# Kernel optimization log

Hardware: AMD Instinct MI355X
Metric: run time of the kernel (lower is better)

Reference implementation:

```python
import jax, jax.numpy as jnp
import numpy as np

T, Q, D, NH, L = 6, 300, 256, 8, 4
DH = D // NH
PC, PT = 2, 1
WT = T - 1
P = PC + WT * PT
DFF = 1024
SHAPES = [(128, 128), (64, 64), (32, 32), (16, 16)]
S_PER_FRAME = sum(h * w for h, w in SHAPES)


def _layer_norm(x, g, b, eps=1e-5):
    mu = jnp.mean(x, -1, keepdims=True)
    v = jnp.mean(jnp.square(x - mu), -1, keepdims=True)
    return (x - mu) * jax.lax.rsqrt(v + eps) * g + b


def _bilinear(vlh, loc, frame_pt, Hl, Wl):
    # vlh: [NH, T*Hl*Wl, DH]; loc: [TQ, NH, P, 2] normalized; frame_pt: np [TQ, P] int32
    x = loc[..., 0] * Wl - 0.5
    y = loc[..., 1] * Hl - 0.5
    x0 = jnp.floor(x)
    y0 = jnp.floor(y)
    fx = x - x0
    fy = y - y0
    x0 = x0.astype(jnp.int32)
    y0 = y0.astype(jnp.int32)
    fbase = (frame_pt[:, None, :] * np.int32(Hl * Wl)).astype(np.int32)  # [TQ,1,P]
    acc = 0.0
    for dy, wy in ((0, 1.0 - fy), (1, fy)):
        for dx, wx in ((0, 1.0 - fx), (1, fx)):
            xi = x0 + dx
            yi = y0 + dy
            ok = (xi >= 0) & (xi < Wl) & (yi >= 0) & (yi < Hl)
            idx = fbase + jnp.clip(yi, 0, Hl - 1) * Wl + jnp.clip(xi, 0, Wl - 1)  # [TQ,NH,P]
            g = jax.vmap(lambda v, i: v[i], in_axes=(0, 1), out_axes=0)(vlh, idx)  # [NH,TQ,P,DH]
            w = wy * wx * ok  # [TQ,NH,P]
            acc = acc + g * jnp.transpose(w, (1, 0, 2))[..., None]
    return acc  # [NH,TQ,P,DH]


def _forward(src, tgt_masks, query_pos, reference_points, src_valid_ratios,
             Wq, bq, Wk, bk, Wv, bv, Wo, bo, norm2_g, norm2_b,
             Wval, bval, Woff, boff, Watt, batt, Wout, bout, norm1_g, norm1_b,
             W1, b1, W2, b2, norm3_g, norm3_b,
             src_spatial_shapes, src_level_start_index):
    shapes = np.asarray(src_spatial_shapes)
    # ---- self-attention across frames (seq=T, batch=Q, as in nn.MultiheadAttention) ----
    qk_in = tgt_masks + query_pos  # [T,Q,D]
    qh = (qk_in @ Wq.T + bq).reshape(T, Q, NH, DH)
    kh = (qk_in @ Wk.T + bk).reshape(T, Q, NH, DH)
    vh = (tgt_masks @ Wv.T + bv).reshape(T, Q, NH, DH)
    logits = jnp.einsum('iqhd,jqhd->qhij', qh, kh) * (1.0 / np.sqrt(DH))
    attn = jax.nn.softmax(logits, -1)
    sa = jnp.einsum('qhij,jqhd->iqhd', attn, vh).reshape(T, Q, D) @ Wo.T + bo
    tgt = _layer_norm(tgt_masks + sa, norm2_g, norm2_b)  # [T,Q,D]

    tgt = tgt.reshape(T * Q, D)
    query = tgt + query_pos.reshape(T * Q, D)

    # ---- current-frame and temporal (same-instance) reference points ----
    ref = reference_points.reshape(T * Q, 2)
    vr0 = src_valid_ratios[0]  # [L,2]
    ref_curr = ref[:, None, :] * vr0[None]  # [TQ,L,2]
    others = np.array([[f for f in range(T) if f != t] for t in range(T)], np.int32)  # [T,WT]
    ref_oth = reference_points[others]  # [T,WT,Q,2]
    ref_oth = jnp.transpose(ref_oth, (0, 2, 1, 3)).reshape(T * Q, WT, 2)
    ref_temp = ref_oth[:, :, None, :] * vr0[None, None]  # [TQ,WT,L,2]

    fid = np.repeat(np.arange(T, dtype=np.int32), Q)  # [TQ]
    oth_fid = np.repeat(others, Q, axis=0)  # [TQ,WT]
    frame_pt = np.concatenate([np.tile(fid[:, None], (1, PC)), oth_fid], axis=1).astype(np.int32)  # [TQ,P]

    # ---- temporal multi-scale deformable cross-attention ----
    value = (src[0] @ Wval.T + bval).reshape(-1, NH, DH)  # [T*S,NH,DH]
    off = (query @ Woff.T + boff).reshape(T * Q, NH, L, P, 2)
    att = jax.nn.softmax((query @ Watt.T + batt).reshape(T * Q, NH, L * P), -1)
    att = att.reshape(T * Q, NH, L, P)

    out = jnp.zeros((T * Q, NH, DH), src.dtype)
    start = 0
    for l in range(L):
        Hl, Wl = int(shapes[l, 0]), int(shapes[l, 1])
        n = T * Hl * Wl
        vlh = value[start:start + n].transpose(1, 0, 2)  # [NH, T*Hl*Wl, DH]
        start += n
        bc = jnp.tile(ref_curr[:, l][:, None, :], (1, PC, 1))  # [TQ,PC,2]
        bt = ref_temp[:, :, l, :]  # [TQ,WT,2]
        base = jnp.concatenate([bc, bt], 1)[:, None]  # [TQ,1,P,2]
        loc = base + off[:, :, l] / jnp.array([Wl, Hl], jnp.float32)  # [TQ,NH,P,2]
        sampled = _bilinear(vlh, loc, frame_pt, Hl, Wl)  # [NH,TQ,P,DH]
        out = out + jnp.einsum('nqpd,qnp->qnd', sampled, att[:, :, l])
    cross = out.reshape(T * Q, D) @ Wout.T + bout
    tgt = _layer_norm(tgt + cross, norm1_g, norm1_b)

    # ---- FFN ----
    h = jax.nn.relu(tgt @ W1.T + b1)
    tgt = _layer_norm(tgt + h @ W2.T + b2, norm3_g, norm3_b)
    return tgt.reshape(T, Q, D)


def setup_inputs() -> dict:
    key = jax.random.key(0)
    ki = iter(jax.random.split(key, 48))

    def rn(shape, s=1.0):
        return jax.random.normal(next(ki), shape, jnp.float32) * s

    return {
        'src': rn((1, T * S_PER_FRAME, D)),
        'tgt_masks': rn((T, Q, D)),
        'query_pos': rn((T, Q, D), 0.5),
        'reference_points': jax.random.uniform(next(ki), (T, Q, 2), jnp.float32, 0.25, 0.75),
        'src_valid_ratios': jax.random.uniform(next(ki), (T, L, 2), jnp.float32, 0.9, 1.0),
        'src_spatial_shapes': jnp.array(SHAPES, jnp.int32),
        'src_level_start_index': jnp.array(np.cumsum([0] + [T * h * w for h, w in SHAPES[:-1]]), jnp.int32),
        'Wq': rn((D, D), 0.02), 'bq': jnp.zeros((D,)),
        'Wk': rn((D, D), 0.02), 'bk': jnp.zeros((D,)),
        'Wv': rn((D, D), 0.02), 'bv': jnp.zeros((D,)),
        'Wo': rn((D, D), 0.02), 'bo': jnp.zeros((D,)),
        'norm2_g': jnp.ones((D,)), 'norm2_b': jnp.zeros((D,)),
        'Wval': rn((D, D), 0.02), 'bval': jnp.zeros((D,)),
        'Woff': rn((NH * L * P * 2, D), 0.01), 'boff': rn((NH * L * P * 2,), 0.1),
        'Watt': rn((NH * L * P, D), 0.01), 'batt': jnp.zeros((NH * L * P,)),
        'Wout': rn((D, D), 0.02), 'bout': jnp.zeros((D,)),
        'norm1_g': jnp.ones((D,)), 'norm1_b': jnp.zeros((D,)),
        'W1': rn((DFF, D), 0.02), 'b1': jnp.zeros((DFF,)),
        'W2': rn((D, DFF), 0.02), 'b2': jnp.zeros((D,)),
        'norm3_g': jnp.ones((D,)), 'norm3_b': jnp.zeros((D,)),
    }


def reference(src, tgt_masks, query_pos, reference_points, src_valid_ratios,
              src_spatial_shapes, src_level_start_index,
              Wq, bq, Wk, bk, Wv, bv, Wo, bo, norm2_g, norm2_b,
              Wval, bval, Woff, boff, Watt, batt, Wout, bout, norm1_g, norm1_b,
              W1, b1, W2, b2, norm3_g, norm3_b):
    return _forward(src, tgt_masks, query_pos, reference_points, src_valid_ratios,
                    Wq, bq, Wk, bk, Wv, bv, Wo, bo, norm2_g, norm2_b,
                    Wval, bval, Woff, boff, Watt, batt, Wout, bout, norm1_g, norm1_b,
                    W1, b1, W2, b2, norm3_g, norm3_b,
                    src_spatial_shapes, src_level_start_index)
```

## Files before the change

### kernel.cpp

```cpp
#include <hip/hip_runtime.h>
#include <hip/hip_bf16.h>

#define T_ 6
#define Q_ 300
#define TQ 1800
#define D_ 256
#define NH_ 8
#define DH_ 32
#define L_ 4
#define P_ 7
#define DFF_ 1024
#define NV 130560
#define NVB 1020
#define QKVB 174

#define OW_VAL 0
#define OW_Q   65536
#define OW_K   131072
#define OW_V   196608
#define OW_O   262144
#define OW_OUT 327680
#define OW_OFF 393216
#define OW_ATT 507904
#define OW_1   565248
#define OW_2   827392
#define OW_TOT 1089536

typedef __attribute__((ext_vector_type(8))) short bf16x8;
typedef __attribute__((ext_vector_type(4))) float f32x4;
typedef __attribute__((ext_vector_type(8))) unsigned short u16x8;
typedef __attribute__((ext_vector_type(4))) unsigned short u16x4;

__device__ inline float bf2f(unsigned short s) {
    union { unsigned u; float f; } v; v.u = ((unsigned)s) << 16;
    return v.f;
}
__device__ inline unsigned short f2b_rn(float f) {
    __hip_bfloat16 h = __float2bfloat16(f);
    union { __hip_bfloat16 h; unsigned short u; } c; c.h = h; return c.u;
}

__global__ __launch_bounds__(256) void wcvt_kernel(
    const float* __restrict__ s0, const float* __restrict__ s1,
    const float* __restrict__ s2, const float* __restrict__ s3,
    const float* __restrict__ s4, const float* __restrict__ s5,
    const float* __restrict__ s6, const float* __restrict__ s7,
    const float* __restrict__ s8, const float* __restrict__ s9,
    unsigned short* __restrict__ dst)
{
    int idx4 = blockIdx.x * blockDim.x + threadIdx.x;
    const int total4 = OW_TOT / 4;
    for (; idx4 < total4; idx4 += gridDim.x * blockDim.x) {
        int e = idx4 * 4;
        const float* s; int off;
        if      (e < OW_Q)   { s = s0; off = e; }
        else if (e < OW_K)   { s = s1; off = e - OW_Q; }
        else if (e < OW_V)   { s = s2; off = e - OW_K; }
        else if (e < OW_O)   { s = s3; off = e - OW_V; }
        else if (e < OW_OUT) { s = s4; off = e - OW_O; }
        else if (e < OW_OFF) { s = s5; off = e - OW_OUT; }
        else if (e < OW_ATT) { s = s6; off = e - OW_OFF; }
        else if (e < OW_1)   { s = s7; off = e - OW_ATT; }
        else if (e < OW_2)   { s = s8; off = e - OW_1; }
        else                 { s = s9; off = e - OW_2; }
        f32x4 v = *(const f32x4*)(s + off);
        u16x4 o;
#pragma unroll
        for (int j = 0; j < 4; j++) o[j] = f2b_rn(v[j]);
        *(u16x4*)(dst + e) = o;
    }
}

__global__ __launch_bounds__(512) void mega1_kernel(
    const float* __restrict__ A, const unsigned short* __restrict__ wbf,
    const float* __restrict__ bias,
    unsigned short* __restrict__ out,
    const float* __restrict__ tgtm, const float* __restrict__ qpos,
    const float* __restrict__ bq, const float* __restrict__ bk,
    const float* __restrict__ bv,
    float* __restrict__ qh, float* __restrict__ kh, float* __restrict__ vh)
{
    __shared__ unsigned short Ws[256 * 256];
    __shared__ float As[2][128 * 32];

    int tid = threadIdx.x;
    int wave = tid >> 6, lane = tid & 63;
    int r = lane & 15, g = lane >> 4;

    if (blockIdx.x < NVB) {
        int m0 = blockIdx.x * 128;
        int rs = r & 7;

#pragma unroll
        for (int j = 0; j < 16; j++) {
            int o = wave * 16 + j;
            int col = o * 2 + (lane >> 5);
            int slot = lane & 31;
            const unsigned short* s =
                wbf + OW_VAL + (size_t)col * 256 + (size_t)((slot ^ (col & 7)) * 8);
            __builtin_amdgcn_global_load_lds(
                (const __attribute__((address_space(1))) void*)s,
                (__attribute__((address_space(3))) void*)&Ws[o * 512], 16, 0, 0);
        }

#define DMA_A(ks, b) do { \
        int o_ = wave * 2; \
        int ro_ = o_ * 8 + (lane >> 3); \
        int kg_ = (lane & 7) ^ (lane >> 3); \
        const float* s0_ = A + (size_t)(m0 + ro_) * 256 + (ks) * 32 + kg_ * 4; \
        const float* s1_ = s0_ + 8 * 256; \
        __builtin_amdgcn_global_load_lds( \
            (const __attribute__((address_space(1))) void*)s0_, \
            (__attribute__((address_space(3))) void*)&As[b][o_ * 256], 16, 0, 0); \
        __builtin_amdgcn_global_load_lds( \
            (const __attribute__((address_space(1))) void*)s1_, \
            (__attribute__((address_space(3))) void*)&As[b][(o_ + 1) * 256], 16, 0, 0); \
    } while (0)

        DMA_A(0, 0);
        __syncthreads();

        int wm = wave >> 2, wn = wave & 3;
        f32x4 acc[4][4] = {};

#define PHASE(ks, b) do { \
        bf16x8 af[4]; \
        _Pragma("unroll") \
        for (int mi = 0; mi < 4; mi++) { \
            int row_ = wm * 64 + mi * 16 + r; \
            f32x4 lo_ = *(const f32x4*)&As[b][row_ * 32 + (((g * 2) ^ rs) << 2)]; \
            f32x4 hi_ = *(const f32x4*)&As[b][row_ * 32 + (((g * 2 + 1) ^ rs) << 2)]; \
            _Pragma("unroll") \
            for (int j = 0; j < 4; j++) { \
                af[mi][j] = (short)f2b_rn(lo_[j]); \
                af[mi][4 + j] = (short)f2b_rn(hi_[j]); \
            } \
        } \
        _Pragma("unroll") \
        for (int ni = 0; ni < 4; ni++) { \
            int col_ = wn * 64 + ni * 16 + r; \
            bf16x8 bfr = *(const bf16x8*)&Ws[col_ * 256 + ((((ks) * 4 + g) ^ rs) << 3)]; \
            _Pragma("unroll") \
            for (int mi = 0; mi < 4; mi++) \
                acc[mi][ni] = __builtin_amdgcn_mfma_f32_16x16x32_bf16(af[mi], bfr, acc[mi][ni], 0, 0, 0); \
        } \
    } while (0)

        DMA_A(1, 1); PHASE(0, 0); __syncthreads();
        DMA_A(2, 0); PHASE(1, 1); __syncthreads();
        DMA_A(3, 1); PHASE(2, 0); __syncthreads();
        DMA_A(4, 0); PHASE(3, 1); __syncthreads();
        DMA_A(5, 1); PHASE(4, 0); __syncthreads();
        DMA_A(6, 0); PHASE(5, 1); __syncthreads();
        DMA_A(7, 1); PHASE(6, 0); __syncthreads();
        PHASE(7, 1);
#undef PHASE
#undef DMA_A

#pragma unroll
        for (int ni = 0; ni < 4; ni++) {
            int col = wn * 64 + ni * 16 + r;
            float bv2 = bias[col];
#pragma unroll
            for (int mi = 0; mi < 4; mi++) {
#pragma unroll
                for (int rr = 0; rr < 4; rr++) {
                    int row = m0 + wm * 64 + mi * 16 + g * 4 + rr;
                    out[(size_t)row * 256 + col] = f2b_rn(acc[mi][ni][rr] + bv2);
                }
            }
        }
    } else {
        int b = blockIdx.x - NVB;
        int bmx = b % 29, by = b / 29;
        int wm = wave >> 2, wn = wave & 3;
        int m0 = bmx * 64 + wm * 32;
        int n0g = by * 128 + wn * 32;
        int seg = n0g >> 8;
        int n0 = n0g & 255;
        const unsigned short* Wp = wbf + (seg == 0 ? OW_Q : (seg == 1 ? OW_K : OW_V));
        const float* bp = (seg == 0) ? bq : (seg == 1) ? bk : bv;
        float* outp = (seg == 0) ? qh : (seg == 1) ? kh : vh;
        bool add2 = (seg < 2);

        f32x4 acc[2][2] = {};
#pragma unroll
        for (int kk = 0; kk < 256; kk += 32) {
            int kbase = kk + g * 8;
            bf16x8 af[2], wf[2];
#pragma unroll
            for (int mi = 0; mi < 2; mi++) {
                int row = m0 + mi * 16 + r; if (row >= TQ) row = TQ - 1;
                const float* ap = tgtm + (size_t)row * 256 + kbase;
                f32x4 lo = *(const f32x4*)ap, hi = *(const f32x4*)(ap + 4);
                if (add2) {
                    const float* ap2 = qpos + (size_t)row * 256 + kbase;
                    lo += *(const f32x4*)ap2; hi += *(const f32x4*)(ap2 + 4);
                }
#pragma unroll
                for (int j = 0; j < 4; j++) { af[mi][j] = (short)f2b_rn(lo[j]); af[mi][4 + j] = (short)f2b_rn(hi[j]); }
            }
#pragma unroll
            for (int ni = 0; ni < 2; ni++) {
                int col = n0 + ni * 16 + r;
                wf[ni] = *(const bf16x8*)&Wp[(size_t)col * 256 + kbase];
            }
#pragma unroll
            for (int mi = 0; mi < 2; mi++)
#pragma unroll
                for (int ni = 0; ni < 2; ni++)
                    acc[mi][ni] = __builtin_amdgcn_mfma_f32_16x16x32_bf16(af[mi], wf[ni], acc[mi][ni], 0, 0, 0);
        }
#pragma unroll
        for (int mi = 0; mi < 2; mi++)
#pragma unroll
            for (int ni = 0; ni < 2; ni++) {
                int col = n0 + ni * 16 + r;
                float bv2 = bp[col];
#pragma unroll
                for (int rr = 0; rr < 4; rr++) {
                    int row = m0 + mi * 16 + g * 4 + rr;
                    if (row < TQ) outp[(size_t)row * 256 + col] = acc[mi][ni][rr] + bv2;
                }
            }
    }
}

__global__ __launch_bounds__(256) void attn_wo_ln2_kernel(
    const float* __restrict__ qh, const float* __restrict__ kh,
    const float* __restrict__ vh, const float* __restrict__ tgtm,
    const float* __restrict__ qpos, const unsigned short* __restrict__ wbf,
    const float* __restrict__ bo, const float* __restrict__ n2g,
    const float* __restrict__ n2b,
    float* __restrict__ tgt1, float* __restrict__ query)
{
    int q = blockIdx.x;
    int tid = threadIdx.x;
    __shared__ float qs[T_][D_], ks_[T_][D_], vs[T_][D_];
    __shared__ unsigned short po[16][268];
    __shared__ float sa32[16][264];

#pragma unroll
    for (int i = 0; i < T_; i++) {
        size_t base = (size_t)(i * Q_ + q) * D_ + tid;
        qs[i][tid] = qh[base]; ks_[i][tid] = kh[base]; vs[i][tid] = vh[base];
    }
    __syncthreads();

    const float scale = 0.17677669529663687f;
    float lg[T_][T_];
#pragma unroll
    for (int i = 0; i < T_; i++)
#pragma unroll
        for (int j = 0; j < T_; j++) {
            float p = qs[i][tid] * ks_[j][tid];
#pragma unroll
            for (int m = 16; m >= 1; m >>= 1) p += __shfl_xor(p, m, 32);
            lg[i][j] = p * scale;
        }
#pragma unroll
    for (int i = 0; i < T_; i++) {
        float mx = lg[i][0];
#pragma unroll
        for (int j = 1; j < T_; j++) mx = fmaxf(mx, lg[i][j]);
        float w[T_]; float sum = 0.f;
#pragma unroll
        for (int j = 0; j < T_; j++) { w[j] = __expf(lg[i][j] - mx); sum += w[j]; }
        float inv = 1.f / sum;
        float a = 0.f;
#pragma unroll
        for (int j = 0; j < T_; j++) a += w[j] * inv * vs[j][tid];
        po[i][tid] = f2b_rn(a);
    }
#pragma unroll
    for (int i = T_; i < 16; i++) po[i][tid] = 0;
    __syncthreads();

    const unsigned short* Wo = wbf + OW_O;
    int wn = tid >> 6, lane = tid & 63;
    int r = lane & 15, g = lane >> 4;
    f32x4 acc[4] = {};
#pragma unroll
    for (int ksx = 0; ksx < 8; ksx++) {
        int kbase = ksx * 32 + g * 8;
        bf16x8 af = *(const bf16x8*)&po[r][kbase];
        bf16x8 bfr[4];
#pragma unroll
        for (int ni = 0; ni < 4; ni++)
            bfr[ni] = *(const bf16x8*)&Wo[(size_t)(wn * 64 + ni * 16 + r) * 256 + kbase];
#pragma unroll
        for (int ni = 0; ni < 4; ni++)
            acc[ni] = __builtin_amdgcn_mfma_f32_16x16x32_bf16(af, bfr[ni], acc[ni], 0, 0, 0);
    }
#pragma unroll
    for (int ni = 0; ni < 4; ni++) {
        int col = wn * 64 + ni * 16 + r;
#pragma unroll
        for (int rr = 0; rr < 4; rr++) {
            int row = g * 4 + rr;
            if (row < T_)
                sa32[row][col] = acc[ni][rr] + bo[col] + tgtm[(size_t)(row * Q_ + q) * 256 + col];
        }
    }
    __syncthreads();

    int rl = tid >> 3, l8 = tid & 7;
    if (rl < T_) {
        float s = 0.f, s2 = 0.f;
#pragma unroll
        for (int c = 0; c < 256; c += 8) {
            float v = sa32[rl][c + l8];
            s += v; s2 += v * v;
        }
#pragma unroll
        for (int m = 4; m >= 1; m >>= 1) { s += __shfl_xor(s, m, 64); s2 += __shfl_xor(s2, m, 64); }
        float mu = s * (1.f / 256.f);
        float var = s2 * (1.f / 256.f) - mu * mu;
        float rs = rsqrtf(var + 1e-5f);
        size_t grow = (size_t)(rl * Q_ + q) * 256;
#pragma unroll
        for (int c = 0; c < 256; c += 8) {
            int cc = c + l8;
            float y = (sa32[rl][cc] - mu) * rs * n2g[cc] + n2b[cc];
            tgt1[grow + cc] = y;
            query[grow + cc] = y + qpos[grow + cc];
        }
    }
}

__global__ __launch_bounds__(256) void offatt_kernel(
    const float* __restrict__ query, const unsigned short* __restrict__ wbf,
    const float* __restrict__ boff, const float* __restrict__ batt,
    float* __restrict__ offb, float* __restrict__ attl)
{
    int wave = threadIdx.x >> 6;
    int lane = threadIdx.x & 63;
    int wm = wave >> 1, wn = wave & 1;
    int m0 = blockIdx.x * 64 + wm * 32;
    int n0g = blockIdx.y * 64 + wn * 32;
    int seg = (n0g >= 448);
    int n0 = seg ? (n0g - 448) : n0g;
    int Nloc = seg ? 224 : 448;
    const unsigned short* W = wbf + (seg ? OW_ATT : OW_OFF);
    const float* bias = seg ? batt : boff;
    float* out = seg ? attl : offb;
    int r = lane & 15, g = lane >> 4;

    f32x4 acc[2][2] = {};
#pragma unroll
    for (int kk = 0; kk < 256; kk += 32) {
        int kbase = kk + g * 8;
        bf16x8 af[2], wf[2];
#pragma unroll
        for (int mi = 0; mi < 2; mi++) {
            int row = m0 + mi * 16 + r; if (row >= TQ) row = TQ - 1;
            const float* ap = query + (size_t)row * 256 + kbase;
            f32x4 lo = *(const f32x4*)ap, hi = *(const f32x4*)(ap + 4);
#pragma unroll
            for (int j = 0; j < 4; j++) { af[mi][j] = (short)f2b_rn(lo[j]); af[mi][4 + j] = (short)f2b_rn(hi[j]); }
        }
#pragma unroll
        for (int ni = 0; ni < 2; ni++) {
            int col = n0 + ni * 16 + r; if (col >= Nloc) col = Nloc - 1;
            wf[ni] = *(const bf16x8*)&W[(size_t)col * 256 + kbase];
        }
#pragma unroll
        for (int mi = 0; mi < 2; mi++)
#pragma unroll
            for (int ni = 0; ni < 2; ni++)
                acc[mi][ni] = __builtin_amdgcn_mfma_f32_16x16x32_bf16(af[mi], wf[ni], acc[mi][ni], 0, 0, 0);
    }
#pragma unroll
    for (int mi = 0; mi < 2; mi++)
#pragma unroll
        for (int ni = 0; ni < 2; ni++) {
            int col = n0 + ni * 16 + r;
            if (col < Nloc) {
                float bv2 = bias[col];
#pragma unroll
                for (int rr = 0; rr < 4; rr++) {
                    int row = m0 + mi * 16 + g * 4 + rr;
                    if (row < TQ) out[(size_t)row * Nloc + col] = acc[mi][ni][rr] + bv2;
                }
            }
        }
}

__global__ __launch_bounds__(256) void sample_kernel(
    const unsigned short* __restrict__ value, const float* __restrict__ attl,
    const float* __restrict__ off, const float* __restrict__ refp,
    const float* __restrict__ vr, float* __restrict__ out)
{
    int q = blockIdx.x;
    int tid = threadIdx.x;
    int d = tid & 31, h = tid >> 5;
    int t = q / Q_, qq = q - t * Q_;

    __shared__ float aw[NH_][28], ofx[NH_][28], ofy[NH_][28];

    float lgv = (d < 28) ? attl[(size_t)q * 224 + h * 28 + d] : -1e30f;
    float mx = lgv;
#pragma unroll
    for (int m = 16; m >= 1; m >>= 1) mx = fmaxf(mx, __shfl_xor(mx, m, 32));
    float e = (d < 28) ? __expf(lgv - mx) : 0.f;
    float s = e;
#pragma unroll
    for (int m = 16; m >= 1; m >>= 1) s += __shfl_xor(s, m, 32);
    if (d < 28) {
        aw[h][d] = e / s;
        ofx[h][d] = off[(size_t)q * 448 + h * 56 + d * 2 + 0];
        ofy[h][d] = off[(size_t)q * 448 + h * 56 + d * 2 + 1];
    }
    __syncthreads();

    const int WLs[4] = {128, 64, 32, 16};
    const int LST[4] = {0, 98304, 122880, 129024};

    float acc = 0.f;
#pragma unroll
    for (int l = 0; l < L_; l++) {
        const int Wl = WLs[l], Hl = WLs[l];
        const int lst = LST[l];
        float vrx = vr[l * 2 + 0], vry = vr[l * 2 + 1];
#pragma unroll
        for (int p = 0; p < P_; p++) {
            int f = (p < 2) ? t : (((p - 2) < t) ? (p - 2) : (p - 1));
            float rx = refp[(size_t)(f * Q_ + qq) * 2 + 0];
            float ry = refp[(size_t)(f * Q_ + qq) * 2 + 1];
            int ip = l * 7 + p;
            float x = rx * vrx * (float)Wl + ofx[h][ip] - 0.5f;
            float y = ry * vry * (float)Hl + ofy[h][ip] - 0.5f;
            float x0f = floorf(x), y0f = floorf(y);
            float fx = x - x0f, fy = y - y0f;
            int x0 = (int)x0f, y0 = (int)y0f;
            int fbase = lst + f * Hl * Wl;
            float a = aw[h][ip];
#pragma unroll
            for (int dy = 0; dy < 2; dy++) {
                int yi = y0 + dy;
                float wy = dy ? fy : 1.f - fy;
                int yc = min(max(yi, 0), Hl - 1);
                bool oky = (yi >= 0) && (yi < Hl);
#pragma unroll
                for (int dx = 0; dx < 2; dx++) {
                    int xi = x0 + dx;
                    float wx = dx ? fx : 1.f - fx;
                    int xc = min(max(xi, 0), Wl - 1);
                    bool ok = oky && (xi >= 0) && (xi < Wl);
                    float v = bf2f(value[((size_t)(fbase + yc * Wl + xc)) * D_ + h * DH_ + d]);
                    acc += a * (ok ? (wy * wx) : 0.f) * v;
                }
            }
        }
    }
    out[(size_t)q * D_ + tid] = acc;
}

__global__ __launch_bounds__(256) void tail_kernel(
    const float* __restrict__ samp, const unsigned short* __restrict__ wbf,
    const float* __restrict__ bout, const float* __restrict__ tgt1,
    const float* __restrict__ n1g, const float* __restrict__ n1b,
    const float* __restrict__ b1, const float* __restrict__ b2,
    const float* __restrict__ n3g, const float* __restrict__ n3b,
    float* __restrict__ dout)
{
    __shared__ float c32[16][264];
    __shared__ float t232[16][264];
    __shared__ unsigned short t2bf[16][268];
    __shared__ unsigned short hbf[16][1036];

    int tid = threadIdx.x;
    int wn = tid >> 6, lane = tid & 63;
    int r = lane & 15, g = lane >> 4;
    int m0 = blockIdx.x * 16;

    const unsigned short* Wout = wbf + OW_OUT;
    const unsigned short* W1 = wbf + OW_1;
    const unsigned short* W2 = wbf + OW_2;

    {
        f32x4 acc[4] = {};
        int row = m0 + r; if (row >= TQ) row = TQ - 1;
#pragma unroll
        for (int ksx = 0; ksx < 8; ksx++) {
            int kbase = ksx * 32 + g * 8;
            const float* ap = samp + (size_t)row * 256 + kbase;
            f32x4 lo = *(const f32x4*)ap, hi = *(const f32x4*)(ap + 4);
            bf16x8 af;
#pragma unroll
            for (int j = 0; j < 4; j++) { af[j] = (short)f2b_rn(lo[j]); af[4 + j] = (short)f2b_rn(hi[j]); }
            bf16x8 bfr[4];
#pragma unroll
            for (int ni = 0; ni < 4; ni++)
                bfr[ni] = *(const bf16x8*)&Wout[(size_t)(wn * 64 + ni * 16 + r) * 256 + kbase];
#pragma unroll
            for (int ni = 0; ni < 4; ni++)
                acc[ni] = __builtin_amdgcn_mfma_f32_16x16x32_bf16(af, bfr[ni], acc[ni], 0, 0, 0);
        }
#pragma unroll
        for (int ni = 0; ni < 4; ni++) {
            int col = wn * 64 + ni * 16 + r;
            float bv = bout[col];
#pragma unroll
            for (int rr = 0; rr < 4; rr++) {
                int rowl = g * 4 + rr;
                int grow = m0 + rowl;
                float res = (grow < TQ) ? tgt1[(size_t)grow * 256 + col] : 0.f;
                c32[rowl][col] = acc[ni][rr] + bv + res;
            }
        }
    }
    __syncthreads();

    if (tid < 128) {
        int rl = tid >> 3, l8 = tid & 7;
        float s = 0.f, s2 = 0.f;
#pragma unroll
        for (int c = 0; c < 256; c += 8) {
            float v = c32[rl][c + l8];
            s += v; s2 += v * v;
        }
#pragma unroll
        for (int m = 4; m >= 1; m >>= 1) { s += __shfl_xor(s, m, 64); s2 += __shfl_xor(s2, m, 64); }
        float mu = s * (1.f / 256.f);
        float var = s2 * (1.f / 256.f) - mu * mu;
        float rs = rsqrtf(var + 1e-5f);
#pragma unroll
        for (int c = 0; c < 256; c += 8) {
            int cc = c + l8;
            float y = (c32[rl][cc] - mu) * rs * n1g[cc] + n1b[cc];
            t232[rl][cc] = y;
            t2bf[rl][cc] = f2b_rn(y);
        }
    }
    __syncthreads();

    {
        f32x4 acc[16] = {};
#pragma unroll
        for (int ksx = 0; ksx < 8; ksx++) {
            int kbase = ksx * 32 + g * 8;
            bf16x8 af = *(const bf16x8*)&t2bf[r][kbase];
#pragma unroll
            for (int ni = 0; ni < 16; ni++) {
                bf16x8 bfr = *(const bf16x8*)&W1[(size_t)(wn * 256 + ni * 16 + r) * 256 + kbase];
                acc[ni] = __builtin_amdgcn_mfma_f32_16x16x32_bf16(af, bfr, acc[ni], 0, 0, 0);
            }
        }
#pragma unroll
        for (int ni = 0; ni < 16; ni++) {
            int col = wn * 256 + ni * 16 + r;
            float bv = b1[col];
#pragma unroll
            for (int rr = 0; rr < 4; rr++) {
                int rowl = g * 4 + rr;
                hbf[rowl][col] = f2b_rn(fmaxf(acc[ni][rr] + bv, 0.f));
            }
        }
    }
    __syncthreads();

    {
        f32x4 acc[4] = {};
#pragma unroll
        for (int ksx = 0; ksx < 32; ksx++) {
            int kbase = ksx * 32 + g * 8;
            bf16x8 af = *(const bf16x8*)&hbf[r][kbase];
#pragma unroll
            for (int ni = 0; ni < 4; ni++) {
                bf16x8 bfr = *(const bf16x8*)&W2[(size_t)(wn * 64 + ni * 16 + r) * 1024 + kbase];
                acc[ni] = __builtin_amdgcn_mfma_f32_16x16x32_bf16(af, bfr, acc[ni], 0, 0, 0);
            }
        }
#pragma unroll
        for (int ni = 0; ni < 4; ni++) {
            int col = wn * 64 + ni * 16 + r;
            float bv = b2[col];
#pragma unroll
            for (int rr = 0; rr < 4; rr++) {
                int rowl = g * 4 + rr;
                c32[rowl][col] = acc[ni][rr] + bv + t232[rowl][col];
            }
        }
    }
    __syncthreads();

    if (tid < 128) {
        int rl = tid >> 3, l8 = tid & 7;
        int grow = m0 + rl;
        if (grow < TQ) {
            float s = 0.f, s2 = 0.f;
#pragma unroll
            for (int c = 0; c < 256; c += 8) {
                float v = c32[rl][c + l8];
                s += v; s2 += v * v;
            }
#pragma unroll
            for (int m = 4; m >= 1; m >>= 1) { s += __shfl_xor(s, m, 64); s2 += __shfl_xor(s2, m, 64); }
            float mu = s * (1.f / 256.f);
            float var = s2 * (1.f / 256.f) - mu * mu;
            float rs = rsqrtf(var + 1e-5f);
#pragma unroll
            for (int c = 0; c < 256; c += 8) {
                int cc = c + l8;
                dout[(size_t)grow * 256 + cc] = (c32[rl][cc] - mu) * rs * n3g[cc] + n3b[cc];
            }
        }
    }
}

extern "C" void kernel_launch(void* const* d_in, const int* in_sizes, int n_in,
                              void* d_out, int out_size, void* d_ws, size_t ws_size,
                              hipStream_t stream) {
    const float* src  = (const float*)d_in[0];
    const float* tgtm = (const float*)d_in[1];
    const float* qpos = (const float*)d_in[2];
    const float* refp = (const float*)d_in[3];
    const float* vr   = (const float*)d_in[4];
    const float* Wq = (const float*)d_in[7];  const float* bq = (const float*)d_in[8];
    const float* Wk = (const float*)d_in[9];  const float* bk = (const float*)d_in[10];
    const float* Wv = (const float*)d_in[11]; const float* bv = (const float*)d_in[12];
    const float* Wo = (const float*)d_in[13]; const float* bo = (const float*)d_in[14];
    const float* n2g = (const float*)d_in[15]; const float* n2b = (const float*)d_in[16];
    const float* Wval = (const float*)d_in[17]; const float* bval = (const float*)d_in[18];
    const float* Woff = (const float*)d_in[19]; const float* boff = (const float*)d_in[20];
    const float* Watt = (const float*)d_in[21]; const float* batt = (const float*)d_in[22];
    const float* Wout = (const float*)d_in[23]; const float* bout = (const float*)d_in[24];
    const float* n1g = (const float*)d_in[25]; const float* n1b = (const float*)d_in[26];
    const float* W1 = (const float*)d_in[27]; const float* b1 = (const float*)d_in[28];
    const float* W2 = (const float*)d_in[29]; const float* b2 = (const float*)d_in[30];
    const float* n3g = (const float*)d_in[31]; const float* n3b = (const float*)d_in[32];

    char* ws = (char*)d_ws;
    size_t o = 0;
    auto alloc = [&](size_t bytes) -> void* {
        void* p = ws + o; o += (bytes + 255) & ~(size_t)255; return p;
    };
    unsigned short* value = (unsigned short*)alloc((size_t)NV * D_ * 2);
    unsigned short* wbf   = (unsigned short*)alloc((size_t)OW_TOT * 2);
    float* qh     = (float*)alloc((size_t)TQ * D_ * 4);
    float* kh     = (float*)alloc((size_t)TQ * D_ * 4);
    float* vh     = (float*)alloc((size_t)TQ * D_ * 4);
    float* tgt1   = (float*)alloc((size_t)TQ * D_ * 4);
    float* query  = (float*)alloc((size_t)TQ * D_ * 4);
    float* offb   = (float*)alloc((size_t)TQ * 448 * 4);
    float* attl   = (float*)alloc((size_t)TQ * 224 * 4);
    float* samp   = (float*)alloc((size_t)TQ * D_ * 4);

    const int MT = (TQ + 63) / 64;

    wcvt_kernel<<<dim3((OW_TOT / 4 + 255) / 256), dim3(256), 0, stream>>>(
        Wval, Wq, Wk, Wv, Wo, Wout, Woff, Watt, W1, W2, wbf);

    mega1_kernel<<<dim3(NVB + QKVB), dim3(512), 0, stream>>>(
        src, wbf, bval, value, tgtm, qpos, bq, bk, bv, qh, kh, vh);

    attn_wo_ln2_kernel<<<dim3(Q_), dim3(256), 0, stream>>>(
        qh, kh, vh, tgtm, qpos, wbf, bo, n2g, n2b, tgt1, query);

    offatt_kernel<<<dim3(MT, 11), dim3(256), 0, stream>>>(query, wbf, boff, batt, offb, attl);

    sample_kernel<<<dim3(TQ), dim3(256), 0, stream>>>(value, attl, offb, refp, vr, samp);

    tail_kernel<<<dim3((TQ + 15) / 16), dim3(256), 0, stream>>>(
        samp, wbf, bout, tgt1, n1g, n1b, b1, b2, n3g, n3b, (float*)d_out);
}
```

Measured before the change: 191.1 us.

## Make value GEMM persistent over four tiles and fuse QKV projection into attention

Result: faster. 183.5 us (-4.0%).

```diff
diff --git a/kernel.cpp b/kernel.cpp
--- a/kernel.cpp
+++ b/kernel.cpp
@@ -11,8 +11,7 @@
 #define P_ 7
 #define DFF_ 1024
 #define NV 130560
-#define NVB 1020
-#define QKVB 174
+#define VBLK 255
 
 #define OW_VAL 0
 #define OW_Q   65536
@@ -71,14 +70,9 @@
     }
 }
 
-__global__ __launch_bounds__(512) void mega1_kernel(
+__global__ __launch_bounds__(512) void vgemm_kernel(
     const float* __restrict__ A, const unsigned short* __restrict__ wbf,
-    const float* __restrict__ bias,
-    unsigned short* __restrict__ out,
-    const float* __restrict__ tgtm, const float* __restrict__ qpos,
-    const float* __restrict__ bq, const float* __restrict__ bk,
-    const float* __restrict__ bv,
-    float* __restrict__ qh, float* __restrict__ kh, float* __restrict__ vh)
+    const float* __restrict__ bias, unsigned short* __restrict__ out)
 {
     __shared__ unsigned short Ws[256 * 256];
     __shared__ float As[2][128 * 32];
@@ -86,28 +80,26 @@
     int tid = threadIdx.x;
     int wave = tid >> 6, lane = tid & 63;
     int r = lane & 15, g = lane >> 4;
-
-    if (blockIdx.x < NVB) {
-        int m0 = blockIdx.x * 128;
-        int rs = r & 7;
-
-#pragma unroll
-        for (int j = 0; j < 16; j++) {
-            int o = wave * 16 + j;
-            int col = o * 2 + (lane >> 5);
-            int slot = lane & 31;
-            const unsigned short* s =
-                wbf + OW_VAL + (size_t)col * 256 + (size_t)((slot ^ (col & 7)) * 8);
-            __builtin_amdgcn_global_load_lds(
-                (const __attribute__((address_space(1))) void*)s,
-                (__attribute__((address_space(3))) void*)&Ws[o * 512], 16, 0, 0);
-        }
-
-#define DMA_A(ks, b) do { \
+    int rs = r & 7;
+    int base_m = blockIdx.x * 512;
+
+#pragma unroll
+    for (int j = 0; j < 16; j++) {
+        int o = wave * 16 + j;
+        int col = o * 2 + (lane >> 5);
+        int slot = lane & 31;
+        const unsigned short* s =
+            wbf + OW_VAL + (size_t)col * 256 + (size_t)((slot ^ (col & 7)) * 8);
+        __builtin_amdgcn_global_load_lds(
+            (const __attribute__((address_space(1))) void*)s,
+            (__attribute__((address_space(3))) void*)&Ws[o * 512], 16, 0, 0);
+    }
+
+#define DMA_A(tile, ks, b) do { \
         int o_ = wave * 2; \
         int ro_ = o_ * 8 + (lane >> 3); \
         int kg_ = (lane & 7) ^ (lane >> 3); \
-        const float* s0_ = A + (size_t)(m0 + ro_) * 256 + (ks) * 32 + kg_ * 4; \
+        const float* s0_ = A + (size_t)(base_m + (tile) * 128 + ro_) * 256 + (ks) * 32 + kg_ * 4; \
         const float* s1_ = s0_ + 8 * 256; \
         __builtin_amdgcn_global_load_lds( \
             (const __attribute__((address_space(1))) void*)s0_, \
@@ -117,125 +109,85 @@
             (__attribute__((address_space(3))) void*)&As[b][(o_ + 1) * 256], 16, 0, 0); \
     } while (0)
 
-        DMA_A(0, 0);
-        __syncthreads();
-
-        int wm = wave >> 2, wn = wave & 3;
-        f32x4 acc[4][4] = {};
-
-#define PHASE(ks, b) do { \
-        bf16x8 af[4]; \
-        _Pragma("unroll") \
-        for (int mi = 0; mi < 4; mi++) { \
-            int row_ = wm * 64 + mi * 16 + r; \
-            f32x4 lo_ = *(const f32x4*)&As[b][row_ * 32 + (((g * 2) ^ rs) << 2)]; \
-            f32x4 hi_ = *(const f32x4*)&As[b][row_ * 32 + (((g * 2 + 1) ^ rs) << 2)]; \
-            _Pragma("unroll") \
-            for (int j = 0; j < 4; j++) { \
-                af[mi][j] = (short)f2b_rn(lo_[j]); \
-                af[mi][4 + j] = (short)f2b_rn(hi_[j]); \
-            } \
-        } \
-        _Pragma("unroll") \
-        for (int ni = 0; ni < 4; ni++) { \
-            int col_ = wn * 64 + ni * 16 + r; \
-            bf16x8 bfr = *(const bf16x8*)&Ws[col_ * 256 + ((((ks) * 4 + g) ^ rs) << 3)]; \
-            _Pragma("unroll") \
-            for (int mi = 0; mi < 4; mi++) \
-                acc[mi][ni] = __builtin_amdgcn_mfma_f32_16x16x32_bf16(af[mi], bfr, acc[mi][ni], 0, 0, 0); \
-        } \
-    } while (0)
-
-        DMA_A(1, 1); PHASE(0, 0); __syncthreads();
-        DMA_A(2, 0); PHASE(1, 1); __syncthreads();
-        DMA_A(3, 1); PHASE(2, 0); __syncthreads();
-        DMA_A(4, 0); PHASE(3, 1); __syncthreads();
-        DMA_A(5, 1); PHASE(4, 0); __syncthreads();
-        DMA_A(6, 0); PHASE(5, 1); __syncthreads();
-        DMA_A(7, 1); PHASE(6, 0); __syncthreads();
-        PHASE(7, 1);
-#undef PHASE
+    DMA_A(0, 0, 0);
+    DMA_A(0, 1, 1);
+
+    int wm = wave >> 2, wn = wave & 3;
+    f32x4 acc[4][4] = {};
+
+    for (int p = 0; p < 32; ++p) {
+        if (p == 31) { asm volatile("s_waitcnt vmcnt(0)" ::: "memory"); }
+        else         { asm volatile("s_waitcnt vmcnt(2)" ::: "memory"); }
+        __builtin_amdgcn_s_barrier();
+        __builtin_amdgcn_sched_barrier(0);
+
+        int tile = p >> 3, ks = p & 7, b = p & 1;
+
+        {
+            bf16x8 af[4];
+#pragma unroll
+            for (int mi = 0; mi < 4; mi++) {
+                int row_ = wm * 64 + mi * 16 + r;
+                f32x4 lo_ = *(const f32x4*)&As[b][row_ * 32 + (((g * 2) ^ rs) << 2)];
+                f32x4 hi_ = *(const f32x4*)&As[b][row_ * 32 + (((g * 2 + 1) ^ rs) << 2)];
+#pragma unroll
+                for (int j = 0; j < 4; j++) {
+                    af[mi][j] = (short)f2b_rn(lo_[j]);
+                    af[mi][4 + j] = (short)f2b_rn(hi_[j]);
+                }
+            }
+#pragma unroll
+            for (int ni = 0; ni < 4; ni++) {
+                int col_ = wn * 64 + ni * 16 + r;
+                bf16x8 bfr = *(const bf16x8*)&Ws[col_ * 256 + (((ks * 4 + g) ^ rs) << 3)];
+#pragma unroll
+                for (int mi = 0; mi < 4; mi++)
+                    acc[mi][ni] = __builtin_amdgcn_mfma_f32_16x16x32_bf16(af[mi], bfr, acc[mi][ni], 0, 0, 0);
+            }
+        }
+
+        __builtin_amdgcn_s_barrier();
+        __builtin_amdgcn_sched_barrier(0);
+
+        int pn = p + 2;
+        if (pn < 32) DMA_A(pn >> 3, pn & 7, b);
+
+        if (ks == 7) {
+            int mbase = base_m + tile * 128 + wm * 64;
+#pragma unroll
+            for (int ni = 0; ni < 4; ni++) {
+                int col = wn * 64 + ni * 16 + r;
+                float bv2 = bias[col];
+#pragma unroll
+                for (int mi = 0; mi < 4; mi++) {
+#pragma unroll
+                    for (int rr = 0; rr < 4; rr++) {
+                        int row = mbase + mi * 16 + g * 4 + rr;
+                        out[(size_t)row * 256 + col] = f2b_rn(acc[mi][ni][rr] + bv2);
+                    }
+                }
+            }
+#pragma unroll
+            for (int mi = 0; mi < 4; mi++)
+#pragma unroll
+                for (int ni = 0; ni < 4; ni++)
+                    acc[mi][ni] = (f32x4){0.f, 0.f, 0.f, 0.f};
+        }
+    }
 #undef DMA_A
-
-#pragma unroll
-        for (int ni = 0; ni < 4; ni++) {
-            int col = wn * 64 + ni * 16 + r;
-            float bv2 = bias[col];
-#pragma unroll
-            for (int mi = 0; mi < 4; mi++) {
-#pragma unroll
-                for (int rr = 0; rr < 4; rr++) {
-                    int row = m0 + wm * 64 + mi * 16 + g * 4 + rr;
-                    out[(size_t)row * 256 + col] = f2b_rn(acc[mi][ni][rr] + bv2);
-                }
-            }
-        }
-    } else {
-        int b = blockIdx.x - NVB;
-        int bmx = b % 29, by = b / 29;
-        int wm = wave >> 2, wn = wave & 3;
-        int m0 = bmx * 64 + wm * 32;
-        int n0g = by * 128 + wn * 32;
-        int seg = n0g >> 8;
-        int n0 = n0g & 255;
-        const unsigned short* Wp = wbf + (seg == 0 ? OW_Q : (seg == 1 ? OW_K : OW_V));
-        const float* bp = (seg == 0) ? bq : (seg == 1) ? bk : bv;
-        float* outp = (seg == 0) ? qh : (seg == 1) ? kh : vh;
-        bool add2 = (seg < 2);
-
-        f32x4 acc[2][2] = {};
-#pragma unroll
-        for (int kk = 0; kk < 256; kk += 32) {
-            int kbase = kk + g * 8;
-            bf16x8 af[2], wf[2];
-#pragma unroll
-            for (int mi = 0; mi < 2; mi++) {
-                int row = m0 + mi * 16 + r; if (row >= TQ) row = TQ - 1;
-                const float* ap = tgtm + (size_t)row * 256 + kbase;
-                f32x4 lo = *(const f32x4*)ap, hi = *(const f32x4*)(ap + 4);
-                if (add2) {
-                    const float* ap2 = qpos + (size_t)row * 256 + kbase;
-                    lo += *(const f32x4*)ap2; hi += *(const f32x4*)(ap2 + 4);
-                }
-#pragma unroll
-                for (int j = 0; j < 4; j++) { af[mi][j] = (short)f2b_rn(lo[j]); af[mi][4 + j] = (short)f2b_rn(hi[j]); }
-            }
-#pragma unroll
-            for (int ni = 0; ni < 2; ni++) {
-                int col = n0 + ni * 16 + r;
-                wf[ni] = *(const bf16x8*)&Wp[(size_t)col * 256 + kbase];
-            }
-#pragma unroll
-            for (int mi = 0; mi < 2; mi++)
-#pragma unroll
-                for (int ni = 0; ni < 2; ni++)
-                    acc[mi][ni] = __builtin_amdgcn_mfma_f32_16x16x32_bf16(af[mi], wf[ni], acc[mi][ni], 0, 0, 0);
-        }
-#pragma unroll
-        for (int mi = 0; mi < 2; mi++)
-#pragma unroll
-            for (int ni = 0; ni < 2; ni++) {
-                int col = n0 + ni * 16 + r;
-                float bv2 = bp[col];
-#pragma unroll
-                for (int rr = 0; rr < 4; rr++) {
-                    int row = m0 + mi * 16 + g * 4 + rr;
-                    if (row < TQ) outp[(size_t)row * 256 + col] = acc[mi][ni][rr] + bv2;
-                }
-            }
-    }
 }
 
 __global__ __launch_bounds__(256) void attn_wo_ln2_kernel(
-    const float* __restrict__ qh, const float* __restrict__ kh,
-    const float* __restrict__ vh, const float* __restrict__ tgtm,
-    const float* __restrict__ qpos, const unsigned short* __restrict__ wbf,
-    const float* __restrict__ bo, const float* __restrict__ n2g,
-    const float* __restrict__ n2b,
+    const float* __restrict__ tgtm, const float* __restrict__ qpos,
+    const unsigned short* __restrict__ wbf,
+    const float* __restrict__ bq, const float* __restrict__ bk,
+    const float* __restrict__ bv, const float* __restrict__ bo,
+    const float* __restrict__ n2g, const float* __restrict__ n2b,
     float* __restrict__ tgt1, float* __restrict__ query)
 {
     int q = blockIdx.x;
     int tid = threadIdx.x;
+    __shared__ unsigned short xq[16][264], xv[16][264];
     __shared__ float qs[T_][D_], ks_[T_][D_], vs[T_][D_];
     __shared__ unsigned short po[16][268];
     __shared__ float sa32[16][264];
@@ -243,7 +195,48 @@
 #pragma unroll
     for (int i = 0; i < T_; i++) {
         size_t base = (size_t)(i * Q_ + q) * D_ + tid;
-        qs[i][tid] = qh[base]; ks_[i][tid] = kh[base]; vs[i][tid] = vh[base];
+        float tv = tgtm[base];
+        xq[i][tid] = f2b_rn(tv + qpos[base]);
+        xv[i][tid] = f2b_rn(tv);
+    }
+#pragma unroll
+    for (int i = T_; i < 16; i++) { xq[i][tid] = 0; xv[i][tid] = 0; }
+    __syncthreads();
+
+    int wn = tid >> 6, lane = tid & 63;
+    int r = lane & 15, g = lane >> 4;
+
+#pragma unroll
+    for (int proj = 0; proj < 3; proj++) {
+        const unsigned short* Wp = wbf + (proj == 0 ? OW_Q : (proj == 1 ? OW_K : OW_V));
+        const float* bp = (proj == 0) ? bq : (proj == 1) ? bk : bv;
+        f32x4 acc[4] = {};
+#pragma unroll
+        for (int ksx = 0; ksx < 8; ksx++) {
+            int kbase = ksx * 32 + g * 8;
+            bf16x8 af = (proj == 2) ? *(const bf16x8*)&xv[r][kbase]
+                                    : *(const bf16x8*)&xq[r][kbase];
+#pragma unroll
+            for (int ni = 0; ni < 4; ni++) {
+                bf16x8 wf = *(const bf16x8*)&Wp[(size_t)(wn * 64 + ni * 16 + r) * 256 + kbase];
+                acc[ni] = __builtin_amdgcn_mfma_f32_16x16x32_bf16(af, wf, acc[ni], 0, 0, 0);
+            }
+        }
+#pragma unroll
+        for (int ni = 0; ni < 4; ni++) {
+            int col = wn * 64 + ni * 16 + r;
+            float bv2 = bp[col];
+#pragma unroll
+            for (int rr = 0; rr < 4; rr++) {
+                int row = g * 4 + rr;
+                if (row < T_) {
+                    float v = acc[ni][rr] + bv2;
+                    if (proj == 0) qs[row][col] = v;
+                    else if (proj == 1) ks_[row][col] = v;
+                    else vs[row][col] = v;
+                }
+            }
+        }
     }
     __syncthreads();
 
@@ -277,8 +270,6 @@
     __syncthreads();
 
     const unsigned short* Wo = wbf + OW_O;
-    int wn = tid >> 6, lane = tid & 63;
-    int r = lane & 15, g = lane >> 4;
     f32x4 acc[4] = {};
 #pragma unroll
     for (int ksx = 0; ksx < 8; ksx++) {
@@ -316,12 +307,12 @@
         for (int m = 4; m >= 1; m >>= 1) { s += __shfl_xor(s, m, 64); s2 += __shfl_xor(s2, m, 64); }
         float mu = s * (1.f / 256.f);
         float var = s2 * (1.f / 256.f) - mu * mu;
-        float rs = rsqrtf(var + 1e-5f);
+        float rsv = rsqrtf(var + 1e-5f);
         size_t grow = (size_t)(rl * Q_ + q) * 256;
 #pragma unroll
         for (int c = 0; c < 256; c += 8) {
             int cc = c + l8;
-            float y = (sa32[rl][cc] - mu) * rs * n2g[cc] + n2b[cc];
+            float y = (sa32[rl][cc] - mu) * rsv * n2g[cc] + n2b[cc];
             tgt1[grow + cc] = y;
             query[grow + cc] = y + qpos[grow + cc];
         }
@@ -638,9 +629,6 @@
     };
     unsigned short* value = (unsigned short*)alloc((size_t)NV * D_ * 2);
     unsigned short* wbf   = (unsigned short*)alloc((size_t)OW_TOT * 2);
-    float* qh     = (float*)alloc((size_t)TQ * D_ * 4);
-    float* kh     = (float*)alloc((size_t)TQ * D_ * 4);
-    float* vh     = (float*)alloc((size_t)TQ * D_ * 4);
     float* tgt1   = (float*)alloc((size_t)TQ * D_ * 4);
     float* query  = (float*)alloc((size_t)TQ * D_ * 4);
     float* offb   = (float*)alloc((size_t)TQ * 448 * 4);
@@ -652,11 +640,10 @@
     wcvt_kernel<<<dim3((OW_TOT / 4 + 255) / 256), dim3(256), 0, stream>>>(
         Wval, Wq, Wk, Wv, Wo, Wout, Woff, Watt, W1, W2, wbf);
 
-    mega1_kernel<<<dim3(NVB + QKVB), dim3(512), 0, stream>>>(
-        src, wbf, bval, value, tgtm, qpos, bq, bk, bv, qh, kh, vh);
+    vgemm_kernel<<<dim3(VBLK), dim3(512), 0, stream>>>(src, wbf, bval, value);
 
     attn_wo_ln2_kernel<<<dim3(Q_), dim3(256), 0, stream>>>(
-        qh, kh, vh, tgtm, qpos, wbf, bo, n2g, n2b, tgt1, query);
+        tgtm, qpos, wbf, bq, bk, bv, bo, n2g, n2b, tgt1, query);
 
     offatt_kernel<<<dim3(MT, 11), dim3(256), 0, stream>>>(query, wbf, boff, batt, offb, attl);
 
```
